# Kernel optimization log

Measured on AMD Instinct MI355X. Metric: run time of the kernel, lower is better.

The kernel has to match this reference:

```python
import jax, jax.numpy as jnp
import numpy as np

B, T, C = 2, 2048, 1024
H = 16
D = C // H  # head_size = 64
FF = 4 * C
EPS = 1e-5


def _layernorm(x, g, b):
    mu = jnp.mean(x, axis=-1, keepdims=True)
    var = jnp.var(x, axis=-1, keepdims=True)
    return (x - mu) * jax.lax.rsqrt(var + EPS) * g + b


def setup_inputs() -> dict:
    key = jax.random.key(0)
    ks = jax.random.split(key, 12)
    s_in = 1.0 / np.sqrt(C)
    s_ff = 1.0 / np.sqrt(FF)
    return {
        "x": jax.random.normal(ks[0], (B, T, C), jnp.float32),
        "Wq": jax.random.uniform(ks[1], (H, C, D), jnp.float32, -s_in, s_in),
        "Wk": jax.random.uniform(ks[2], (H, C, D), jnp.float32, -s_in, s_in),
        "Wv": jax.random.uniform(ks[3], (H, C, D), jnp.float32, -s_in, s_in),
        "Wo": jax.random.uniform(ks[4], (C, C), jnp.float32, -s_in, s_in),
        "bo": jax.random.uniform(ks[5], (C,), jnp.float32, -s_in, s_in),
        "W1": jax.random.uniform(ks[6], (C, FF), jnp.float32, -s_in, s_in),
        "b1": jax.random.uniform(ks[7], (FF,), jnp.float32, -s_in, s_in),
        "W2": jax.random.uniform(ks[8], (FF, C), jnp.float32, -s_ff, s_ff),
        "b2": jax.random.uniform(ks[9], (C,), jnp.float32, -s_ff, s_ff),
        "g1": jnp.ones((C,), jnp.float32),
        "be1": jnp.zeros((C,), jnp.float32),
        "g2": jnp.ones((C,), jnp.float32),
        "be2": jnp.zeros((C,), jnp.float32),
    }


def reference(x, Wq, Wk, Wv, Wo, bo, W1, b1, W2, b2, g1, be1, g2, be2):
    h = _layernorm(x, g1, be1)
    # per-head projections (no bias), vectorized over heads
    q = jnp.einsum("btc,hcd->bhtd", h, Wq)
    k = jnp.einsum("btc,hcd->bhtd", h, Wk)
    v = jnp.einsum("btc,hcd->bhtd", h, Wv)
    # NOTE: original scales by n_embd**-0.5 (C, not head_size) -- faithful
    scores = jnp.einsum("bhtd,bhsd->bhts", q, k) * (C ** -0.5)
    causal = jnp.tril(jnp.ones((T, T), bool))
    scores = jnp.where(causal, scores, -jnp.inf)
    att = jax.nn.softmax(scores, axis=-1)
    out = jnp.einsum("bhts,bhsd->bhtd", att, v)
    out = out.transpose(0, 2, 1, 3).reshape(B, T, C)  # concat heads
    x = out @ Wo + bo + x  # attn residual (dropout=0 -> identity)
    h2 = _layernorm(x, g2, be2)
    ff = jax.nn.relu(h2 @ W1 + b1) @ W2 + b2
    return x + ff
```

## Files before the change

kernel.cpp:

```cpp
#include <hip/hip_runtime.h>
#include <stdint.h>

typedef unsigned short ushort_t;
typedef __attribute__((ext_vector_type(8))) short bf16x8;
typedef __attribute__((ext_vector_type(4))) float f32x4;

__device__ __forceinline__ unsigned short f2b(float f) {
  unsigned u = __float_as_uint(f);
  u += 0x7fffu + ((u >> 16) & 1u);
  return (unsigned short)(u >> 16);
}

__device__ __forceinline__ void async16(const void* g, void* l) {
  __builtin_amdgcn_global_load_lds(
      (const __attribute__((address_space(1))) void*)g,
      (__attribute__((address_space(3))) void*)l, 16, 0, 0);
}

__global__ __launch_bounds__(256) void ln_kernel(
    const float* __restrict__ x, const float* __restrict__ g,
    const float* __restrict__ be, ushort_t* __restrict__ out) {
  const int C = 1024;
  int row = blockIdx.x;
  const float4* xr = (const float4*)(x + (size_t)row * C);
  int tid = threadIdx.x;
  float4 v = xr[tid];
  float s = v.x + v.y + v.z + v.w;
  float sq = v.x * v.x + v.y * v.y + v.z * v.z + v.w * v.w;
  #pragma unroll
  for (int off = 32; off > 0; off >>= 1) {
    s += __shfl_xor(s, off);
    sq += __shfl_xor(sq, off);
  }
  __shared__ float ss[4], ssq[4];
  int wv = tid >> 6;
  if ((tid & 63) == 0) { ss[wv] = s; ssq[wv] = sq; }
  __syncthreads();
  s = ss[0] + ss[1] + ss[2] + ss[3];
  sq = ssq[0] + ssq[1] + ssq[2] + ssq[3];
  float mu = s * (1.f / C);
  float var = sq * (1.f / C) - mu * mu;
  float rs = rsqrtf(var + 1e-5f);
  float4 gv = ((const float4*)g)[tid];
  float4 bv = ((const float4*)be)[tid];
  ushort4 o;
  o.x = f2b((v.x - mu) * rs * gv.x + bv.x);
  o.y = f2b((v.y - mu) * rs * gv.y + bv.y);
  o.z = f2b((v.z - mu) * rs * gv.z + bv.z);
  o.w = f2b((v.w - mu) * rs * gv.w + bv.w);
  ((ushort4*)(out + (size_t)row * C))[tid] = o;
}

__global__ __launch_bounds__(256) void transpose_cast_kernel(
    const float* __restrict__ in, ushort_t* __restrict__ out, int R, int Cin) {
  __shared__ float tile[32][33];
  int bz = blockIdx.z;
  in += (size_t)bz * R * Cin;
  out += (size_t)bz * R * Cin;
  int c0 = blockIdx.x * 32, r0 = blockIdx.y * 32;
  int tx = threadIdx.x, ty = threadIdx.y;
  #pragma unroll
  for (int i = 0; i < 4; i++)
    tile[ty + 8 * i][tx] = in[(size_t)(r0 + ty + 8 * i) * Cin + c0 + tx];
  __syncthreads();
  #pragma unroll
  for (int i = 0; i < 4; i++)
    out[(size_t)(c0 + ty + 8 * i) * R + r0 + tx] = f2b(tile[tx][ty + 8 * i]);
}

__global__ __launch_bounds__(256) void transpose_v_kernel(
    const ushort_t* __restrict__ qkv, ushort_t* __restrict__ vt) {
  __shared__ ushort_t tile[32][33];
  int bh = blockIdx.z;
  int b = bh >> 4, h = bh & 15;
  int d0 = blockIdx.x * 32, t0 = blockIdx.y * 32;
  int tx = threadIdx.x, ty = threadIdx.y;
  #pragma unroll
  for (int i = 0; i < 4; i++)
    tile[ty + 8 * i][tx] =
        qkv[(size_t)(b * 2048 + t0 + ty + 8 * i) * 3072 + 2048 + h * 64 + d0 + tx];
  __syncthreads();
  #pragma unroll
  for (int i = 0; i < 4; i++)
    vt[(size_t)(bh * 64 + d0 + ty + 8 * i) * 2048 + t0 + tx] = tile[tx][ty + 8 * i];
}

template <int N, int K, int FLAGS>
__global__ __launch_bounds__(256, 2) void gemm_bt_kernel(
    const ushort_t* __restrict__ A, const ushort_t* __restrict__ Bt,
    const float* __restrict__ bias, const float* __restrict__ resid,
    void* __restrict__ outv) {
  __shared__ ushort_t Als[128 * 32];
  __shared__ ushort_t Bls[128 * 32];
  int tid = threadIdx.x, w = tid >> 6, lane = tid & 63, quad = lane >> 4, l16 = lane & 15;
  int bn0 = blockIdx.x * 128, bm0 = blockIdx.y * 128;
  int wm = (w >> 1) * 64, wn = (w & 1) * 64;
  f32x4 acc[4][4];
  #pragma unroll
  for (int i = 0; i < 4; i++)
    #pragma unroll
    for (int j = 0; j < 4; j++) acc[i][j] = f32x4{0.f, 0.f, 0.f, 0.f};
  const ushort_t* Ag = A + (size_t)bm0 * K;
  const ushort_t* Bg = Bt + (size_t)bn0 * K;
  int c0 = w * 128 + lane;
  int r0s = c0 >> 2, co0 = (c0 & 3) * 8;
  int c1 = c0 + 64;
  int r1s = c1 >> 2, co1 = (c1 & 3) * 8;
  for (int k0 = 0; k0 < K; k0 += 32) {
    async16(Ag + (size_t)r0s * K + k0 + co0, &Als[w * 1024]);
    async16(Bg + (size_t)r0s * K + k0 + co0, &Bls[w * 1024]);
    async16(Ag + (size_t)r1s * K + k0 + co1, &Als[w * 1024 + 512]);
    async16(Bg + (size_t)r1s * K + k0 + co1, &Bls[w * 1024 + 512]);
    __syncthreads();
    bf16x8 af[4], bf[4];
    #pragma unroll
    for (int i = 0; i < 4; i++)
      af[i] = *(const bf16x8*)&Als[(wm + i * 16 + l16) * 32 + quad * 8];
    #pragma unroll
    for (int j = 0; j < 4; j++)
      bf[j] = *(const bf16x8*)&Bls[(wn + j * 16 + l16) * 32 + quad * 8];
    #pragma unroll
    for (int i = 0; i < 4; i++)
      #pragma unroll
      for (int j = 0; j < 4; j++)
        acc[i][j] = __builtin_amdgcn_mfma_f32_16x16x32_bf16(af[i], bf[j], acc[i][j], 0, 0, 0);
    __syncthreads();
  }
  #pragma unroll
  for (int i = 0; i < 4; i++)
    #pragma unroll
    for (int j = 0; j < 4; j++)
      #pragma unroll
      for (int r = 0; r < 4; r++) {
        int row = bm0 + wm + i * 16 + quad * 4 + r;
        int col = bn0 + wn + j * 16 + l16;
        float v = acc[i][j][r];
        if constexpr (FLAGS & 4) v += bias[col];
        if constexpr (FLAGS & 8) v += resid[(size_t)row * N + col];
        if constexpr (FLAGS & 1) v = fmaxf(v, 0.f);
        if constexpr ((FLAGS & 2) != 0)
          ((ushort_t*)outv)[(size_t)row * N + col] = f2b(v);
        else
          ((float*)outv)[(size_t)row * N + col] = v;
      }
}

__global__ __launch_bounds__(256) void attn_kernel(
    const ushort_t* __restrict__ qkv, const ushort_t* __restrict__ vt,
    ushort_t* __restrict__ out) {
  const int T = 2048, CC = 3072;
  __shared__ ushort_t Kls[2 * 64 * 32];
  __shared__ ushort_t Vls[2 * 64 * 32];
  int fid = blockIdx.x;
  int xslot = fid & 7, inner = fid >> 3;
  int bh = xslot * 4 + (inner & 3);
  int qb = 15 - (inner >> 2);
  int b = bh >> 4, h = bh & 15;
  int q0 = qb * 128;
  int tid = threadIdx.x, w = tid >> 6, lane = tid & 63, quad = lane >> 4, l16 = lane & 15;
  int cc = w * 64 + lane;
  int srow = cc >> 2;
  int sco = (lane & 3) * 8;
  const ushort_t* kg = qkv + (size_t)(b * T + srow) * CC + 1024 + h * 64 + sco;
  const ushort_t* vg = vt + (size_t)(bh * 64 + srow) * T + sco;
  ushort_t* kl = &Kls[(size_t)w * 512];
  ushort_t* vl = &Vls[(size_t)w * 512];
  bf16x8 aq[2][2];
  f32x4 O[2][4];
  float mrun[2] = {-1e30f, -1e30f}, lrun[2] = {0.f, 0.f};
  int q0s[2], trow[2];
  #pragma unroll
  for (int si = 0; si < 2; si++) {
    int s = w + si * 4;
    q0s[si] = q0 + s * 16;
    trow[si] = q0s[si] + l16;
    const ushort_t* qp = qkv + (size_t)(b * T + q0s[si] + l16) * CC + h * 64 + quad * 8;
    aq[si][0] = *(const bf16x8*)qp;
    aq[si][1] = *(const bf16x8*)(qp + 32);
    #pragma unroll
    for (int i = 0; i < 4; i++) O[si][i] = f32x4{0.f, 0.f, 0.f, 0.f};
  }
  int src0 = (quad & 1) * 32 + l16;
  int src1 = src0 + 16;
  bool hiq = quad >= 2;
  int kbmax = (q0 + 127) >> 6;
  for (int kb = 0; kb <= kbmax; kb++) {
    int s0 = kb * 64;
    async16(kg + (size_t)s0 * CC, kl);
    async16(kg + (size_t)s0 * CC + 32, kl + 2048);
    async16(vg + s0, vl);
    async16(vg + s0 + 32, vl + 2048);
    __syncthreads();
    bf16x8 kfr[4][2], vfr[4][2];
    #pragma unroll
    for (int t = 0; t < 4; t++)
      #pragma unroll
      for (int ks = 0; ks < 2; ks++) {
        kfr[t][ks] = *(const bf16x8*)&Kls[(ks * 64 + t * 16 + l16) * 32 + quad * 8];
        vfr[t][ks] = *(const bf16x8*)&Vls[(ks * 64 + t * 16 + l16) * 32 + quad * 8];
      }
    #pragma unroll
    for (int si = 0; si < 2; si++) {
      if (s0 > q0s[si]) continue;
      f32x4 st[4];
      #pragma unroll
      for (int t = 0; t < 4; t++) {
        st[t] = f32x4{0.f, 0.f, 0.f, 0.f};
        #pragma unroll
        for (int ks = 0; ks < 2; ks++)
          st[t] = __builtin_amdgcn_mfma_f32_16x16x32_bf16(kfr[t][ks], aq[si][ks], st[t], 0, 0, 0);
      }
      bool diag = (kb == (q0s[si] >> 6));
      float sv[4][4];
      float vmax = -1e30f;
      #pragma unroll
      for (int t = 0; t < 4; t++)
        #pragma unroll
        for (int r = 0; r < 4; r++) {
          float sc = st[t][r] * 0.03125f;
          int scol = s0 + t * 16 + quad * 4 + r;
          if (diag && scol > trow[si]) sc = -1e30f;
          sv[t][r] = sc;
          vmax = fmaxf(vmax, sc);
        }
      vmax = fmaxf(vmax, __shfl_xor(vmax, 16));
      vmax = fmaxf(vmax, __shfl_xor(vmax, 32));
      float mnew = fmaxf(mrun[si], vmax);
      float alpha = __expf(mrun[si] - mnew);
      mrun[si] = mnew;
      float psum = 0.f;
      int pk[4][2];
      #pragma unroll
      for (int t = 0; t < 4; t++) {
        float p0 = __expf(sv[t][0] - mnew);
        float p1 = __expf(sv[t][1] - mnew);
        float p2 = __expf(sv[t][2] - mnew);
        float p3 = __expf(sv[t][3] - mnew);
        psum += (p0 + p1) + (p2 + p3);
        pk[t][0] = (int)((unsigned)f2b(p0) | ((unsigned)f2b(p1) << 16));
        pk[t][1] = (int)((unsigned)f2b(p2) | ((unsigned)f2b(p3) << 16));
      }
      psum += __shfl_xor(psum, 16);
      psum += __shfl_xor(psum, 32);
      lrun[si] = lrun[si] * alpha + psum;
      #pragma unroll
      for (int dt = 0; dt < 4; dt++) O[si][dt] *= alpha;
      #pragma unroll
      for (int g32 = 0; g32 < 2; g32++) {
        int t0 = 2 * g32, t1 = t0 + 1;
        int a0 = __shfl(pk[t0][0], src0), b0 = __shfl(pk[t1][0], src0);
        int a1 = __shfl(pk[t0][1], src0), b1 = __shfl(pk[t1][1], src0);
        int a2 = __shfl(pk[t0][0], src1), b2 = __shfl(pk[t1][0], src1);
        int a3 = __shfl(pk[t0][1], src1), b3 = __shfl(pk[t1][1], src1);
        union { int4 i; bf16x8 h; } u;
        u.i.x = hiq ? b0 : a0;
        u.i.y = hiq ? b1 : a1;
        u.i.z = hiq ? b2 : a2;
        u.i.w = hiq ? b3 : a3;
        #pragma unroll
        for (int dt = 0; dt < 4; dt++)
          O[si][dt] = __builtin_amdgcn_mfma_f32_16x16x32_bf16(vfr[dt][g32], u.h, O[si][dt], 0, 0, 0);
      }
    }
    __syncthreads();
  }
  #pragma unroll
  for (int si = 0; si < 2; si++) {
    float inv = 1.f / lrun[si];
    #pragma unroll
    for (int dt = 0; dt < 4; dt++) {
      ushort4 o;
      unsigned short* op = (unsigned short*)&o;
      #pragma unroll
      for (int r = 0; r < 4; r++) op[r] = f2b(O[si][dt][r] * inv);
      *(ushort4*)&out[(size_t)(b * T + trow[si]) * 1024 + h * 64 + dt * 16 + quad * 4] = o;
    }
  }
}

extern "C" void kernel_launch(void* const* d_in, const int* in_sizes, int n_in,
                              void* d_out, int out_size, void* d_ws, size_t ws_size,
                              hipStream_t stream) {
  const int B = 2, T = 2048, C = 1024, H = 16, D = 64, FF = 4096;
  const int M = B * T;
  const float* x   = (const float*)d_in[0];
  const float* Wq  = (const float*)d_in[1];
  const float* Wk  = (const float*)d_in[2];
  const float* Wv  = (const float*)d_in[3];
  const float* Wo  = (const float*)d_in[4];
  const float* bo  = (const float*)d_in[5];
  const float* W1  = (const float*)d_in[6];
  const float* b1  = (const float*)d_in[7];
  const float* W2  = (const float*)d_in[8];
  const float* b2  = (const float*)d_in[9];
  const float* g1  = (const float*)d_in[10];
  const float* be1 = (const float*)d_in[11];
  const float* g2  = (const float*)d_in[12];
  const float* be2 = (const float*)d_in[13];
  float* out = (float*)d_out;

  char* ws = (char*)d_ws;
  size_t off = 0;
  auto alloc = [&](size_t bytes) {
    void* p = ws + off;
    off += (bytes + 255) & ~(size_t)255;
    return p;
  };
  ushort_t* qkvt = (ushort_t*)alloc((size_t)3 * C * C * 2);
  ushort_t* wot  = (ushort_t*)alloc((size_t)C * C * 2);
  ushort_t* w1t  = (ushort_t*)alloc((size_t)FF * C * 2);
  ushort_t* w2t  = (ushort_t*)alloc((size_t)C * FF * 2);
  ushort_t* hbuf = (ushort_t*)alloc((size_t)M * C * 2);
  ushort_t* big  = (ushort_t*)alloc((size_t)M * FF * 2);
  ushort_t* vtb  = (ushort_t*)alloc((size_t)M * C * 2);
  ushort_t* aout = (ushort_t*)alloc((size_t)M * C * 2);
  float*    x2   = (float*)alloc((size_t)M * C * 4);

  dim3 tb(32, 8);
  transpose_cast_kernel<<<dim3(D / 32, C / 32, H), tb, 0, stream>>>(Wq, qkvt, C, D);
  transpose_cast_kernel<<<dim3(D / 32, C / 32, H), tb, 0, stream>>>(Wk, qkvt + (size_t)C * C, C, D);
  transpose_cast_kernel<<<dim3(D / 32, C / 32, H), tb, 0, stream>>>(Wv, qkvt + (size_t)2 * C * C, C, D);
  transpose_cast_kernel<<<dim3(C / 32, C / 32, 1), tb, 0, stream>>>(Wo, wot, C, C);
  transpose_cast_kernel<<<dim3(FF / 32, C / 32, 1), tb, 0, stream>>>(W1, w1t, C, FF);
  transpose_cast_kernel<<<dim3(C / 32, FF / 32, 1), tb, 0, stream>>>(W2, w2t, FF, C);
  ln_kernel<<<M, 256, 0, stream>>>(x, g1, be1, hbuf);
  gemm_bt_kernel<3072, 1024, 2><<<dim3(3072 / 128, M / 128), 256, 0, stream>>>(
      hbuf, qkvt, nullptr, nullptr, big);
  transpose_v_kernel<<<dim3(2, T / 32, B * H), tb, 0, stream>>>(big, vtb);
  attn_kernel<<<512, 256, 0, stream>>>(big, vtb, aout);
  gemm_bt_kernel<1024, 1024, 4 | 8><<<dim3(1024 / 128, M / 128), 256, 0, stream>>>(
      aout, wot, bo, x, x2);
  ln_kernel<<<M, 256, 0, stream>>>(x2, g2, be2, hbuf);
  gemm_bt_kernel<4096, 1024, 1 | 2 | 4><<<dim3(4096 / 128, M / 128), 256, 0, stream>>>(
      hbuf, w1t, b1, nullptr, big);
  gemm_bt_kernel<1024, 4096, 4 | 8><<<dim3(1024 / 128, M / 128), 256, 0, stream>>>(
      big, w2t, b2, x2, out);
}
```

Baseline: 408.8 us.

## Double-buffer K/V tiles and halve attention query block per workgroup

The attention kernel now processes 64 query rows per block instead of 128, with one 16-row strip per wave, and launches 1024 blocks. K/V tiles are double-buffered in LDS so the next tile's async load is issued while the current one is computed, which removes one barrier per iteration. The softmax switches to exp2 with log2(e) folded into the scale, and causal masking is applied only on the diagonal tile. Together these aim to hide load latency and raise occupancy, at the cost of more LDS per block and reloading K/V across more blocks.

```diff
diff --git a/kernel.cpp b/kernel.cpp
--- a/kernel.cpp
+++ b/kernel.cpp
@@ -145,136 +145,133 @@
       }
 }
 
-__global__ __launch_bounds__(256) void attn_kernel(
+__global__ __launch_bounds__(256, 4) void attn_kernel(
     const ushort_t* __restrict__ qkv, const ushort_t* __restrict__ vt,
     ushort_t* __restrict__ out) {
   const int T = 2048, CC = 3072;
-  __shared__ ushort_t Kls[2 * 64 * 32];
-  __shared__ ushort_t Vls[2 * 64 * 32];
+  __shared__ ushort_t Kls[2][2 * 64 * 32];
+  __shared__ ushort_t Vls[2][2 * 64 * 32];
   int fid = blockIdx.x;
-  int xslot = fid & 7, inner = fid >> 3;
-  int bh = xslot * 4 + (inner & 3);
-  int qb = 15 - (inner >> 2);
+  int bh = (fid & 7) * 4 + ((fid >> 3) & 3);
+  int qb = 31 - (fid >> 5);
   int b = bh >> 4, h = bh & 15;
-  int q0 = qb * 128;
+  int q0 = qb * 64;
   int tid = threadIdx.x, w = tid >> 6, lane = tid & 63, quad = lane >> 4, l16 = lane & 15;
-  int cc = w * 64 + lane;
-  int srow = cc >> 2;
+  int srow = w * 16 + (lane >> 2);
   int sco = (lane & 3) * 8;
   const ushort_t* kg = qkv + (size_t)(b * T + srow) * CC + 1024 + h * 64 + sco;
   const ushort_t* vg = vt + (size_t)(bh * 64 + srow) * T + sco;
-  ushort_t* kl = &Kls[(size_t)w * 512];
-  ushort_t* vl = &Vls[(size_t)w * 512];
-  bf16x8 aq[2][2];
-  f32x4 O[2][4];
-  float mrun[2] = {-1e30f, -1e30f}, lrun[2] = {0.f, 0.f};
-  int q0s[2], trow[2];
-  #pragma unroll
-  for (int si = 0; si < 2; si++) {
-    int s = w + si * 4;
-    q0s[si] = q0 + s * 16;
-    trow[si] = q0s[si] + l16;
-    const ushort_t* qp = qkv + (size_t)(b * T + q0s[si] + l16) * CC + h * 64 + quad * 8;
-    aq[si][0] = *(const bf16x8*)qp;
-    aq[si][1] = *(const bf16x8*)(qp + 32);
-    #pragma unroll
-    for (int i = 0; i < 4; i++) O[si][i] = f32x4{0.f, 0.f, 0.f, 0.f};
-  }
+  int q0s = q0 + w * 16;
+  int trow = q0s + l16;
+  const ushort_t* qp = qkv + (size_t)(b * T + trow) * CC + h * 64 + quad * 8;
+  bf16x8 aq[2] = { *(const bf16x8*)qp, *(const bf16x8*)(qp + 32) };
+  f32x4 O[4];
+  #pragma unroll
+  for (int i = 0; i < 4; i++) O[i] = f32x4{0.f, 0.f, 0.f, 0.f};
+  float mrun = -1e30f, lrun = 0.f;
+  const float ksc = 0.03125f * 1.44269504f;
   int src0 = (quad & 1) * 32 + l16;
   int src1 = src0 + 16;
   bool hiq = quad >= 2;
-  int kbmax = (q0 + 127) >> 6;
-  for (int kb = 0; kb <= kbmax; kb++) {
+  auto stage = [&](int kb, int bi) {
     int s0 = kb * 64;
-    async16(kg + (size_t)s0 * CC, kl);
-    async16(kg + (size_t)s0 * CC + 32, kl + 2048);
-    async16(vg + s0, vl);
-    async16(vg + s0 + 32, vl + 2048);
+    async16(kg + (size_t)s0 * CC, &Kls[bi][w * 512]);
+    async16(kg + (size_t)s0 * CC + 32, &Kls[bi][2048 + w * 512]);
+    async16(vg + s0, &Vls[bi][w * 512]);
+    async16(vg + s0 + 32, &Vls[bi][2048 + w * 512]);
+  };
+  stage(0, 0);
+  for (int kb = 0; kb <= qb; kb++) {
     __syncthreads();
+    if (kb < qb) stage(kb + 1, (kb + 1) & 1);
+    int bi = kb & 1;
+    int s0 = kb * 64;
     bf16x8 kfr[4][2], vfr[4][2];
     #pragma unroll
     for (int t = 0; t < 4; t++)
       #pragma unroll
       for (int ks = 0; ks < 2; ks++) {
-        kfr[t][ks] = *(const bf16x8*)&Kls[(ks * 64 + t * 16 + l16) * 32 + quad * 8];
-        vfr[t][ks] = *(const bf16x8*)&Vls[(ks * 64 + t * 16 + l16) * 32 + quad * 8];
+        kfr[t][ks] = *(const bf16x8*)&Kls[bi][(ks * 64 + t * 16 + l16) * 32 + quad * 8];
+        vfr[t][ks] = *(const bf16x8*)&Vls[bi][(ks * 64 + t * 16 + l16) * 32 + quad * 8];
       }
-    #pragma unroll
-    for (int si = 0; si < 2; si++) {
-      if (s0 > q0s[si]) continue;
-      f32x4 st[4];
-      #pragma unroll
-      for (int t = 0; t < 4; t++) {
-        st[t] = f32x4{0.f, 0.f, 0.f, 0.f};
-        #pragma unroll
-        for (int ks = 0; ks < 2; ks++)
-          st[t] = __builtin_amdgcn_mfma_f32_16x16x32_bf16(kfr[t][ks], aq[si][ks], st[t], 0, 0, 0);
-      }
-      bool diag = (kb == (q0s[si] >> 6));
-      float sv[4][4];
-      float vmax = -1e30f;
+    f32x4 st[4];
+    #pragma unroll
+    for (int t = 0; t < 4; t++) {
+      st[t] = f32x4{0.f, 0.f, 0.f, 0.f};
+      #pragma unroll
+      for (int ks = 0; ks < 2; ks++)
+        st[t] = __builtin_amdgcn_mfma_f32_16x16x32_bf16(kfr[t][ks], aq[ks], st[t], 0, 0, 0);
+    }
+    float sv[4][4];
+    float vmax = -1e30f;
+    if (kb == qb) {
       #pragma unroll
       for (int t = 0; t < 4; t++)
         #pragma unroll
         for (int r = 0; r < 4; r++) {
-          float sc = st[t][r] * 0.03125f;
+          float sc = st[t][r] * ksc;
           int scol = s0 + t * 16 + quad * 4 + r;
-          if (diag && scol > trow[si]) sc = -1e30f;
+          if (scol > trow) sc = -1e30f;
           sv[t][r] = sc;
           vmax = fmaxf(vmax, sc);
         }
-      vmax = fmaxf(vmax, __shfl_xor(vmax, 16));
-      vmax = fmaxf(vmax, __shfl_xor(vmax, 32));
-      float mnew = fmaxf(mrun[si], vmax);
-      float alpha = __expf(mrun[si] - mnew);
-      mrun[si] = mnew;
-      float psum = 0.f;
-      int pk[4][2];
-      #pragma unroll
-      for (int t = 0; t < 4; t++) {
-        float p0 = __expf(sv[t][0] - mnew);
-        float p1 = __expf(sv[t][1] - mnew);
-        float p2 = __expf(sv[t][2] - mnew);
-        float p3 = __expf(sv[t][3] - mnew);
-        psum += (p0 + p1) + (p2 + p3);
-        pk[t][0] = (int)((unsigned)f2b(p0) | ((unsigned)f2b(p1) << 16));
-        pk[t][1] = (int)((unsigned)f2b(p2) | ((unsigned)f2b(p3) << 16));
-      }
-      psum += __shfl_xor(psum, 16);
-      psum += __shfl_xor(psum, 32);
-      lrun[si] = lrun[si] * alpha + psum;
-      #pragma unroll
-      for (int dt = 0; dt < 4; dt++) O[si][dt] *= alpha;
-      #pragma unroll
-      for (int g32 = 0; g32 < 2; g32++) {
-        int t0 = 2 * g32, t1 = t0 + 1;
-        int a0 = __shfl(pk[t0][0], src0), b0 = __shfl(pk[t1][0], src0);
-        int a1 = __shfl(pk[t0][1], src0), b1 = __shfl(pk[t1][1], src0);
-        int a2 = __shfl(pk[t0][0], src1), b2 = __shfl(pk[t1][0], src1);
-        int a3 = __shfl(pk[t0][1], src1), b3 = __shfl(pk[t1][1], src1);
-        union { int4 i; bf16x8 h; } u;
-        u.i.x = hiq ? b0 : a0;
-        u.i.y = hiq ? b1 : a1;
-        u.i.z = hiq ? b2 : a2;
-        u.i.w = hiq ? b3 : a3;
+    } else {
+      #pragma unroll
+      for (int t = 0; t < 4; t++)
         #pragma unroll
-        for (int dt = 0; dt < 4; dt++)
-          O[si][dt] = __builtin_amdgcn_mfma_f32_16x16x32_bf16(vfr[dt][g32], u.h, O[si][dt], 0, 0, 0);
-      }
+        for (int r = 0; r < 4; r++) {
+          float sc = st[t][r] * ksc;
+          sv[t][r] = sc;
+          vmax = fmaxf(vmax, sc);
+        }
     }
-    __syncthreads();
+    vmax = fmaxf(vmax, __shfl_xor(vmax, 16));
+    vmax = fmaxf(vmax, __shfl_xor(vmax, 32));
+    float mnew = fmaxf(mrun, vmax);
+    float alpha = __builtin_amdgcn_exp2f(mrun - mnew);
+    mrun = mnew;
+    float psum = 0.f;
+    int pk[4][2];
+    #pragma unroll
+    for (int t = 0; t < 4; t++) {
+      float p0 = __builtin_amdgcn_exp2f(sv[t][0] - mnew);
+      float p1 = __builtin_amdgcn_exp2f(sv[t][1] - mnew);
+      float p2 = __builtin_amdgcn_exp2f(sv[t][2] - mnew);
+      float p3 = __builtin_amdgcn_exp2f(sv[t][3] - mnew);
+      psum += (p0 + p1) + (p2 + p3);
+      pk[t][0] = (int)((unsigned)f2b(p0) | ((unsigned)f2b(p1) << 16));
+      pk[t][1] = (int)((unsigned)f2b(p2) | ((unsigned)f2b(p3) << 16));
+    }
+    psum += __shfl_xor(psum, 16);
+    psum += __shfl_xor(psum, 32);
+    lrun = lrun * alpha + psum;
+    #pragma unroll
+    for (int dt = 0; dt < 4; dt++) O[dt] *= alpha;
+    #pragma unroll
+    for (int g32 = 0; g32 < 2; g32++) {
+      int t0 = 2 * g32, t1 = t0 + 1;
+      int a0 = __shfl(pk[t0][0], src0), b0 = __shfl(pk[t1][0], src0);
+      int a1 = __shfl(pk[t0][1], src0), b1 = __shfl(pk[t1][1], src0);
+      int a2 = __shfl(pk[t0][0], src1), b2 = __shfl(pk[t1][0], src1);
+      int a3 = __shfl(pk[t0][1], src1), b3 = __shfl(pk[t1][1], src1);
+      union { int4 i; bf16x8 h; } u;
+      u.i.x = hiq ? b0 : a0;
+      u.i.y = hiq ? b1 : a1;
+      u.i.z = hiq ? b2 : a2;
+      u.i.w = hiq ? b3 : a3;
+      #pragma unroll
+      for (int dt = 0; dt < 4; dt++)
+        O[dt] = __builtin_amdgcn_mfma_f32_16x16x32_bf16(vfr[dt][g32], u.h, O[dt], 0, 0, 0);
+    }
   }
-  #pragma unroll
-  for (int si = 0; si < 2; si++) {
-    float inv = 1.f / lrun[si];
-    #pragma unroll
-    for (int dt = 0; dt < 4; dt++) {
-      ushort4 o;
-      unsigned short* op = (unsigned short*)&o;
-      #pragma unroll
-      for (int r = 0; r < 4; r++) op[r] = f2b(O[si][dt][r] * inv);
-      *(ushort4*)&out[(size_t)(b * T + trow[si]) * 1024 + h * 64 + dt * 16 + quad * 4] = o;
-    }
+  float inv = 1.f / lrun;
+  #pragma unroll
+  for (int dt = 0; dt < 4; dt++) {
+    ushort4 o;
+    unsigned short* op = (unsigned short*)&o;
+    #pragma unroll
+    for (int r = 0; r < 4; r++) op[r] = f2b(O[dt][r] * inv);
+    *(ushort4*)&out[(size_t)(b * T + trow) * 1024 + h * 64 + dt * 16 + quad * 4] = o;
   }
 }
 
@@ -327,7 +324,7 @@
   gemm_bt_kernel<3072, 1024, 2><<<dim3(3072 / 128, M / 128), 256, 0, stream>>>(
       hbuf, qkvt, nullptr, nullptr, big);
   transpose_v_kernel<<<dim3(2, T / 32, B * H), tb, 0, stream>>>(big, vtb);
-  attn_kernel<<<512, 256, 0, stream>>>(big, vtb, aout);
+  attn_kernel<<<1024, 256, 0, stream>>>(big, vtb, aout);
   gemm_bt_kernel<1024, 1024, 4 | 8><<<dim3(1024 / 128, M / 128), 256, 0, stream>>>(
       aout, wot, bo, x, x2);
   ln_kernel<<<M, 256, 0, stream>>>(x2, g2, be2, hbuf);
```

Measured after the change: 373.4 us. 1.09x faster.
